# Performance work log

Hardware: AMD Instinct MI355X
Metric: run time of the kernel (lower is better)

The kernel has to match this reference:

```python
import jax, jax.numpy as jnp
import numpy as np

N = 1_000_000          # number of query points
POINT_DIMS = 2         # (x, y) coordinates
NUM_EMB = 6572         # number of video frames
EMB_DIM = 32
HIDDEN = 128


def setup_inputs() -> dict:
    key = jax.random.key(0)
    ks = jax.random.split(key, 10)
    x = jax.random.uniform(ks[0], (N, POINT_DIMS), dtype=jnp.float32)
    # fractional frame index in [0, NUM_EMB - 1)
    embeddings = jax.random.uniform(ks[1], (N,), dtype=jnp.float32) * (NUM_EMB - 1)
    em_table = jax.random.normal(ks[2], (NUM_EMB, EMB_DIM), dtype=jnp.float32) * 0.1
    in0 = POINT_DIMS + EMB_DIM
    W0 = jax.random.normal(ks[3], (in0, HIDDEN), dtype=jnp.float32) / np.sqrt(in0)
    b0 = jax.random.normal(ks[4], (HIDDEN,), dtype=jnp.float32) * 0.01
    W1 = jax.random.normal(ks[5], (HIDDEN, HIDDEN), dtype=jnp.float32) / np.sqrt(HIDDEN)
    b1 = jax.random.normal(ks[6], (HIDDEN,), dtype=jnp.float32) * 0.01
    W2 = jax.random.normal(ks[7], (HIDDEN, 1), dtype=jnp.float32) / np.sqrt(HIDDEN)
    b2 = jax.random.normal(ks[8], (1,), dtype=jnp.float32) * 0.01
    return {"x": x, "embeddings": embeddings, "em_table": em_table,
            "W0": W0, "b0": b0, "W1": W1, "b1": b1, "W2": W2, "b2": b2}


def reference(x, embeddings, em_table, W0, b0, W1, b1, W2, b2):
    num_emb = em_table.shape[0]
    em1 = embeddings.astype(jnp.int32)                       # floor (inputs >= 0)
    em2 = jnp.minimum(em1 + 1, num_emb - 1)                  # clamp(em1+1, max=E-1)
    res = (embeddings - em1.astype(jnp.float32))[:, None]    # [N, 1]
    e1 = em_table[em1]                                       # [N, 32] gather
    e2 = em_table[em2]                                       # [N, 32] gather
    em = e1 + (e2 - e1) * res                                # lerp
    h = jnp.concatenate((x, em), axis=1) @ W0 + b0           # [N, 128]
    h = jnp.clip(h, 0.0, 1.0)
    h = jnp.clip(h @ W1 + b1, 0.0, 1.0)
    out = jax.nn.sigmoid(h @ W2 + b2)                        # [N, 1]
    return out
```

## Files before the change

### kernel.cpp

```cpp
#include <hip/hip_runtime.h>
#include <hip/hip_bf16.h>


using bf16x8 = __attribute__((ext_vector_type(8))) short;
using f32x4  = __attribute__((ext_vector_type(4))) float;

#define NPTS    1000000
#define NUMEMB  6572
#define HID     128
#define M_IT    64
#define A0S     72
#define H0S     136
#define TILES   (NPTS / M_IT)
#define NBLOCKS 1024

__device__ __forceinline__ unsigned short bf16r(float f) {
    unsigned u;
    __builtin_memcpy(&u, &f, 4);
    u = (u + 0x7fffu + ((u >> 16) & 1u)) >> 16;
    return (unsigned short)u;
}
__device__ __forceinline__ unsigned pk2(float a, float b) {
    float2 f2; f2.x = a; f2.y = b;
    __hip_bfloat162 h = __float22bfloat162_rn(f2);
    unsigned u;
    __builtin_memcpy(&u, &h, 4);
    return u;
}
__device__ __forceinline__ float clamp01(float x) {
    return __builtin_amdgcn_fmed3f(x, 0.f, 1.f);
}

__global__ __launch_bounds__(256, 4)
void mlp_fused(const float* __restrict__ x,
               const float* __restrict__ emb,
               const float* __restrict__ em_table,
               const float* __restrict__ W0, const float* __restrict__ b0,
               const float* __restrict__ W1, const float* __restrict__ b1,
               const float* __restrict__ W2, const float* __restrict__ b2,
               float* __restrict__ out)
{
    __shared__ __align__(16) unsigned short A0[2 * M_IT * A0S];
    __shared__ __align__(16) unsigned short H0[M_IT * H0S];
    __shared__ __align__(16) float PART[16][65];

    const int tid  = threadIdx.x;
    const int lane = tid & 63;
    const int nq   = tid >> 6;
    const int q    = lane >> 4;
    const int cl   = lane & 15;
    const int p    = tid >> 2;
    const int s    = tid & 3;

    for (int i = tid; i < 2 * M_IT * A0S; i += 256) A0[i] = 0;

    const int hcol = nq * 32 + (cl >> 2) * 8 + (cl & 3);
    bf16x8 w0t[2][2];
    for (int hb = 0; hb < 2; ++hb)
        for (int kt = 0; kt < 2; ++kt) {
            const int col = hcol + hb * 4;
            bf16x8 v;
            #pragma unroll
            for (int e = 0; e < 8; ++e) {
                const int k = kt * 32 + q * 8 + e;
                float val = 0.f;
                if (k < 32)       val = W0[(2 + k) * HID + col];
                else if (k == 32) val = W0[0 * HID + col];
                else if (k == 33) val = W0[1 * HID + col];
                v[e] = (short)bf16r(val);
            }
            w0t[hb][kt] = v;
        }

    bf16x8 w1r[2][4];
    for (int hb = 0; hb < 2; ++hb)
        for (int kk = 0; kk < 4; ++kk) {
            const int kt  = (nq + kk) & 3;
            const int col = hcol + hb * 4;
            bf16x8 v;
            #pragma unroll
            for (int e = 0; e < 8; ++e) {
                const int k = kt * 32 + q * 8 + e;
                v[e] = (short)bf16r(W1[k * HID + col]);
            }
            w1r[hb][kk] = v;
        }

    f32x4 b0q[2], b1q[2], w2q[2];
    for (int hb = 0; hb < 2; ++hb)
        for (int r = 0; r < 4; ++r) {
            const int h = nq * 32 + q * 8 + hb * 4 + r;
            b0q[hb][r] = b0[h];
            b1q[hb][r] = b1[h];
            w2q[hb][r] = W2[h];
        }
    const float bias2 = b2[0];

    int t = blockIdx.x;
    int cur = 0;
    {
        const int gp = t * M_IT + p;
        const float fe = emb[gp];
        float2 xv = {0.f, 0.f};
        if (s == 0) xv = *(const float2*)(x + 2 * gp);
        const int e1 = (int)fe;
        const int e2 = (e1 + 1 < NUMEMB) ? e1 + 1 : NUMEMB - 1;
        const float r = fe - (float)e1;
        const float4* p1 = (const float4*)(em_table + e1 * 32 + s * 8);
        const float4* p2 = (const float4*)(em_table + e2 * 32 + s * 8);
        const float4 g0 = p1[0], g1 = p1[1], g2 = p2[0], g3 = p2[1];
        uint4 d;
        d.x = pk2(g0.x + (g2.x - g0.x) * r, g0.y + (g2.y - g0.y) * r);
        d.y = pk2(g0.z + (g2.z - g0.z) * r, g0.w + (g2.w - g0.w) * r);
        d.z = pk2(g1.x + (g3.x - g1.x) * r, g1.y + (g3.y - g1.y) * r);
        d.w = pk2(g1.z + (g3.z - g1.z) * r, g1.w + (g3.w - g1.w) * r);
        *(uint4*)&A0[p * A0S + s * 8] = d;
        if (s == 0) *(unsigned*)&A0[p * A0S + 32] = pk2(xv.x, xv.y);
    }
    float  feB;
    float2 xvB = {0.f, 0.f};
    {
        int t1 = t + gridDim.x; if (t1 >= TILES) t1 = t;
        const int gp = t1 * M_IT + p;
        feB = emb[gp];
        if (s == 0) xvB = *(const float2*)(x + 2 * gp);
    }

    __syncthreads();

    for (; t < TILES; t += gridDim.x, cur ^= 1) {
        const int base = t * M_IT;
        const unsigned short* A0c = A0 + cur * (M_IT * A0S);
        unsigned short*       A0n = A0 + (cur ^ 1) * (M_IT * A0S);

        f32x4 acc[4][2];
        #pragma unroll
        for (int pb = 0; pb < 4; ++pb) {
            #pragma unroll
            for (int kt = 0; kt < 2; ++kt) {
                bf16x8 bfrag = *(const bf16x8*)
                    &A0c[(pb * 16 + cl) * A0S + kt * 32 + q * 8];
                #pragma unroll
                for (int hb = 0; hb < 2; ++hb)
                    acc[pb][hb] = __builtin_amdgcn_mfma_f32_16x16x32_bf16(
                        w0t[hb][kt], bfrag,
                        (kt == 0) ? b0q[hb] : acc[pb][hb], 0, 0, 0);
            }
        }

        const int ge1 = (int)feB;
        const int ge2 = (ge1 + 1 < NUMEMB) ? ge1 + 1 : NUMEMB - 1;
        const float4* gp1 = (const float4*)(em_table + ge1 * 32 + s * 8);
        const float4* gp2 = (const float4*)(em_table + ge2 * 32 + s * 8);
        const float4 g0 = gp1[0], g1 = gp1[1], g2 = gp2[0], g3 = gp2[1];

        uint4 own[4];
        #pragma unroll
        for (int pb = 0; pb < 4; ++pb) {
            const f32x4 v0 = acc[pb][0], v1 = acc[pb][1];
            uint4 w;
            w.x = pk2(clamp01(v0[0]), clamp01(v0[1]));
            w.y = pk2(clamp01(v0[2]), clamp01(v0[3]));
            w.z = pk2(clamp01(v1[0]), clamp01(v1[1]));
            w.w = pk2(clamp01(v1[2]), clamp01(v1[3]));
            own[pb] = w;
            *(uint4*)&H0[(pb * 16 + cl) * H0S + nq * 32 + q * 8] = w;
        }

        {
            const float r = feB - (float)ge1;
            uint4 d;
            d.x = pk2(g0.x + (g2.x - g0.x) * r, g0.y + (g2.y - g0.y) * r);
            d.y = pk2(g0.z + (g2.z - g0.z) * r, g0.w + (g2.w - g0.w) * r);
            d.z = pk2(g1.x + (g3.x - g1.x) * r, g1.y + (g3.y - g1.y) * r);
            d.w = pk2(g1.z + (g3.z - g1.z) * r, g1.w + (g3.w - g1.w) * r);
            *(uint4*)&A0n[p * A0S + s * 8] = d;
            if (s == 0) *(unsigned*)&A0n[p * A0S + 32] = pk2(xvB.x, xvB.y);
        }
        {
            int t2 = t + 2 * (int)gridDim.x; if (t2 >= TILES) t2 = t;
            const int gp = t2 * M_IT + p;
            feB = emb[gp];
            if (s == 0) xvB = *(const float2*)(x + 2 * gp);
        }
        __syncthreads();

        #pragma unroll
        for (int pb = 0; pb < 4; ++pb) {
            bf16x8 bfrag;
            __builtin_memcpy(&bfrag, &own[pb], 16);
            #pragma unroll
            for (int hb = 0; hb < 2; ++hb)
                acc[pb][hb] = __builtin_amdgcn_mfma_f32_16x16x32_bf16(
                    w1r[hb][0], bfrag, b1q[hb], 0, 0, 0);
        }
        #pragma unroll
        for (int kk = 1; kk < 4; ++kk) {
            const int kcol = (((nq + kk) & 3) << 5) + q * 8;
            #pragma unroll
            for (int pb = 0; pb < 4; ++pb) {
                bf16x8 bfrag = *(const bf16x8*)
                    &H0[(pb * 16 + cl) * H0S + kcol];
                #pragma unroll
                for (int hb = 0; hb < 2; ++hb)
                    acc[pb][hb] = __builtin_amdgcn_mfma_f32_16x16x32_bf16(
                        w1r[hb][kk], bfrag, acc[pb][hb], 0, 0, 0);
            }
        }

        #pragma unroll
        for (int pb = 0; pb < 4; ++pb) {
            float sum = 0.f;
            #pragma unroll
            for (int hb = 0; hb < 2; ++hb) {
                const f32x4 v = acc[pb][hb];
                sum += clamp01(v[0]) * w2q[hb][0];
                sum += clamp01(v[1]) * w2q[hb][1];
                sum += clamp01(v[2]) * w2q[hb][2];
                sum += clamp01(v[3]) * w2q[hb][3];
            }
            PART[nq * 4 + q][pb * 16 + cl] = sum;
        }
        __syncthreads();

        if (tid < 64) {
            float z = bias2;
            #pragma unroll
            for (int i = 0; i < 16; ++i) z += PART[i][tid];
            out[base + tid] = 1.f / (1.f + __expf(-z));
        }
    }
}

extern "C" void kernel_launch(void* const* d_in, const int* in_sizes, int n_in,
                              void* d_out, int out_size, void* d_ws, size_t ws_size,
                              hipStream_t stream) {
    const float* x   = (const float*)d_in[0];
    const float* emb = (const float*)d_in[1];
    const float* emt = (const float*)d_in[2];
    const float* W0  = (const float*)d_in[3];
    const float* b0  = (const float*)d_in[4];
    const float* W1  = (const float*)d_in[5];
    const float* b1  = (const float*)d_in[6];
    const float* W2  = (const float*)d_in[7];
    const float* b2  = (const float*)d_in[8];
    mlp_fused<<<NBLOCKS, 256, 0, stream>>>(x, emb, emt, W0, b0, W1, b1, W2, b2,
                                           (float*)d_out);
}
```

Baseline: 133.5 us.

## Double per-block tile to 128 points and halve grid size

Grows each block's tile from 64 to 128 points. Every wave now runs 8 point-blocks per tile, which doubles the MFMA work done between barriers and amortises the per-tile sync and weight-register setup. The grid drops to 512 blocks and occupancy is lowered to 2 blocks per CU to fit the larger accumulators and LDS. Bounds clamping handles the partial last tile. The risk is higher register pressure and fewer resident waves to hide gather latency.

```diff
diff --git a/kernel.cpp b/kernel.cpp
--- a/kernel.cpp
+++ b/kernel.cpp
@@ -8,11 +8,11 @@
 #define NPTS    1000000
 #define NUMEMB  6572
 #define HID     128
-#define M_IT    64
+#define M_IT    128
 #define A0S     72
 #define H0S     136
-#define TILES   (NPTS / M_IT)
-#define NBLOCKS 1024
+#define TILES   ((NPTS + M_IT - 1) / M_IT)
+#define NBLOCKS 512
 
 __device__ __forceinline__ unsigned short bf16r(float f) {
     unsigned u;
@@ -31,7 +31,25 @@
     return __builtin_amdgcn_fmed3f(x, 0.f, 1.f);
 }
 
-__global__ __launch_bounds__(256, 4)
+__device__ __forceinline__ void stage_one(unsigned short* dst,
+                                          const float* __restrict__ em_table,
+                                          float fe, float2 xv, int s) {
+    const int e1 = (int)fe;
+    const int e2 = (e1 + 1 < NUMEMB) ? e1 + 1 : NUMEMB - 1;
+    const float r = fe - (float)e1;
+    const float4* p1 = (const float4*)(em_table + e1 * 32 + s * 8);
+    const float4* p2 = (const float4*)(em_table + e2 * 32 + s * 8);
+    const float4 g0 = p1[0], g1 = p1[1], g2 = p2[0], g3 = p2[1];
+    uint4 d;
+    d.x = pk2(g0.x + (g2.x - g0.x) * r, g0.y + (g2.y - g0.y) * r);
+    d.y = pk2(g0.z + (g2.z - g0.z) * r, g0.w + (g2.w - g0.w) * r);
+    d.z = pk2(g1.x + (g3.x - g1.x) * r, g1.y + (g3.y - g1.y) * r);
+    d.w = pk2(g1.z + (g3.z - g1.z) * r, g1.w + (g3.w - g1.w) * r);
+    *(uint4*)(dst + s * 8) = d;
+    if (s == 0) *(unsigned*)(dst + 32) = pk2(xv.x, xv.y);
+}
+
+__global__ __launch_bounds__(256, 2)
 void mlp_fused(const float* __restrict__ x,
                const float* __restrict__ emb,
                const float* __restrict__ em_table,
@@ -42,7 +60,7 @@
 {
     __shared__ __align__(16) unsigned short A0[2 * M_IT * A0S];
     __shared__ __align__(16) unsigned short H0[M_IT * H0S];
-    __shared__ __align__(16) float PART[16][65];
+    __shared__ __align__(16) float PART[16][M_IT + 1];
 
     const int tid  = threadIdx.x;
     const int lane = tid & 63;
@@ -99,31 +117,24 @@
     int t = blockIdx.x;
     int cur = 0;
     {
-        const int gp = t * M_IT + p;
-        const float fe = emb[gp];
-        float2 xv = {0.f, 0.f};
-        if (s == 0) xv = *(const float2*)(x + 2 * gp);
-        const int e1 = (int)fe;
-        const int e2 = (e1 + 1 < NUMEMB) ? e1 + 1 : NUMEMB - 1;
-        const float r = fe - (float)e1;
-        const float4* p1 = (const float4*)(em_table + e1 * 32 + s * 8);
-        const float4* p2 = (const float4*)(em_table + e2 * 32 + s * 8);
-        const float4 g0 = p1[0], g1 = p1[1], g2 = p2[0], g3 = p2[1];
-        uint4 d;
-        d.x = pk2(g0.x + (g2.x - g0.x) * r, g0.y + (g2.y - g0.y) * r);
-        d.y = pk2(g0.z + (g2.z - g0.z) * r, g0.w + (g2.w - g0.w) * r);
-        d.z = pk2(g1.x + (g3.x - g1.x) * r, g1.y + (g3.y - g1.y) * r);
-        d.w = pk2(g1.z + (g3.z - g1.z) * r, g1.w + (g3.w - g1.w) * r);
-        *(uint4*)&A0[p * A0S + s * 8] = d;
-        if (s == 0) *(unsigned*)&A0[p * A0S + 32] = pk2(xv.x, xv.y);
+        int gp0 = t * M_IT + p;        if (gp0 >= NPTS) gp0 = NPTS - 1;
+        int gp1 = t * M_IT + 64 + p;   if (gp1 >= NPTS) gp1 = NPTS - 1;
+        const float fe0 = emb[gp0], fe1 = emb[gp1];
+        float2 xv0 = {0.f, 0.f}, xv1 = {0.f, 0.f};
+        if (s == 0) { xv0 = *(const float2*)(x + 2 * gp0);
+                      xv1 = *(const float2*)(x + 2 * gp1); }
+        stage_one(&A0[p * A0S], em_table, fe0, xv0, s);
+        stage_one(&A0[(64 + p) * A0S], em_table, fe1, xv1, s);
     }
-    float  feB;
-    float2 xvB = {0.f, 0.f};
+    float  feB0, feB1;
+    float2 xvB0 = {0.f, 0.f}, xvB1 = {0.f, 0.f};
     {
         int t1 = t + gridDim.x; if (t1 >= TILES) t1 = t;
-        const int gp = t1 * M_IT + p;
-        feB = emb[gp];
-        if (s == 0) xvB = *(const float2*)(x + 2 * gp);
+        int gp0 = t1 * M_IT + p;      if (gp0 >= NPTS) gp0 = NPTS - 1;
+        int gp1 = t1 * M_IT + 64 + p; if (gp1 >= NPTS) gp1 = NPTS - 1;
+        feB0 = emb[gp0]; feB1 = emb[gp1];
+        if (s == 0) { xvB0 = *(const float2*)(x + 2 * gp0);
+                      xvB1 = *(const float2*)(x + 2 * gp1); }
     }
 
     __syncthreads();
@@ -133,9 +144,9 @@
         const unsigned short* A0c = A0 + cur * (M_IT * A0S);
         unsigned short*       A0n = A0 + (cur ^ 1) * (M_IT * A0S);
 
-        f32x4 acc[4][2];
-        #pragma unroll
-        for (int pb = 0; pb < 4; ++pb) {
+        f32x4 acc[8][2];
+        #pragma unroll
+        for (int pb = 0; pb < 8; ++pb) {
             #pragma unroll
             for (int kt = 0; kt < 2; ++kt) {
                 bf16x8 bfrag = *(const bf16x8*)
@@ -148,15 +159,15 @@
             }
         }
 
-        const int ge1 = (int)feB;
+        const int ge1 = (int)feB0;
         const int ge2 = (ge1 + 1 < NUMEMB) ? ge1 + 1 : NUMEMB - 1;
-        const float4* gp1 = (const float4*)(em_table + ge1 * 32 + s * 8);
-        const float4* gp2 = (const float4*)(em_table + ge2 * 32 + s * 8);
-        const float4 g0 = gp1[0], g1 = gp1[1], g2 = gp2[0], g3 = gp2[1];
-
-        uint4 own[4];
-        #pragma unroll
-        for (int pb = 0; pb < 4; ++pb) {
+        const float4* gp1p = (const float4*)(em_table + ge1 * 32 + s * 8);
+        const float4* gp2p = (const float4*)(em_table + ge2 * 32 + s * 8);
+        const float4 g0 = gp1p[0], g1 = gp1p[1], g2 = gp2p[0], g3 = gp2p[1];
+
+        uint4 own[8];
+        #pragma unroll
+        for (int pb = 0; pb < 8; ++pb) {
             const f32x4 v0 = acc[pb][0], v1 = acc[pb][1];
             uint4 w;
             w.x = pk2(clamp01(v0[0]), clamp01(v0[1]));
@@ -168,25 +179,29 @@
         }
 
         {
-            const float r = feB - (float)ge1;
+            const float r = feB0 - (float)ge1;
             uint4 d;
             d.x = pk2(g0.x + (g2.x - g0.x) * r, g0.y + (g2.y - g0.y) * r);
             d.y = pk2(g0.z + (g2.z - g0.z) * r, g0.w + (g2.w - g0.w) * r);
             d.z = pk2(g1.x + (g3.x - g1.x) * r, g1.y + (g3.y - g1.y) * r);
             d.w = pk2(g1.z + (g3.z - g1.z) * r, g1.w + (g3.w - g1.w) * r);
             *(uint4*)&A0n[p * A0S + s * 8] = d;
-            if (s == 0) *(unsigned*)&A0n[p * A0S + 32] = pk2(xvB.x, xvB.y);
-        }
+            if (s == 0) *(unsigned*)&A0n[p * A0S + 32] = pk2(xvB0.x, xvB0.y);
+        }
+        stage_one(&A0n[(64 + p) * A0S], em_table, feB1, xvB1, s);
+
         {
             int t2 = t + 2 * (int)gridDim.x; if (t2 >= TILES) t2 = t;
-            const int gp = t2 * M_IT + p;
-            feB = emb[gp];
-            if (s == 0) xvB = *(const float2*)(x + 2 * gp);
+            int gp0 = t2 * M_IT + p;      if (gp0 >= NPTS) gp0 = NPTS - 1;
+            int gpb = t2 * M_IT + 64 + p; if (gpb >= NPTS) gpb = NPTS - 1;
+            feB0 = emb[gp0]; feB1 = emb[gpb];
+            if (s == 0) { xvB0 = *(const float2*)(x + 2 * gp0);
+                          xvB1 = *(const float2*)(x + 2 * gpb); }
         }
         __syncthreads();
 
         #pragma unroll
-        for (int pb = 0; pb < 4; ++pb) {
+        for (int pb = 0; pb < 8; ++pb) {
             bf16x8 bfrag;
             __builtin_memcpy(&bfrag, &own[pb], 16);
             #pragma unroll
@@ -198,7 +213,7 @@
         for (int kk = 1; kk < 4; ++kk) {
             const int kcol = (((nq + kk) & 3) << 5) + q * 8;
             #pragma unroll
-            for (int pb = 0; pb < 4; ++pb) {
+            for (int pb = 0; pb < 8; ++pb) {
                 bf16x8 bfrag = *(const bf16x8*)
                     &H0[(pb * 16 + cl) * H0S + kcol];
                 #pragma unroll
@@ -209,7 +224,7 @@
         }
 
         #pragma unroll
-        for (int pb = 0; pb < 4; ++pb) {
+        for (int pb = 0; pb < 8; ++pb) {
             float sum = 0.f;
             #pragma unroll
             for (int hb = 0; hb < 2; ++hb) {
@@ -223,11 +238,14 @@
         }
         __syncthreads();
 
-        if (tid < 64) {
-            float z = bias2;
-            #pragma unroll
-            for (int i = 0; i < 16; ++i) z += PART[i][tid];
-            out[base + tid] = 1.f / (1.f + __expf(-z));
+        if (tid < 128) {
+            const int gp = base + tid;
+            if (gp < NPTS) {
+                float z = bias2;
+                #pragma unroll
+                for (int i = 0; i < 16; ++i) z += PART[i][tid];
+                out[gp] = 1.f / (1.f + __expf(-z));
+            }
         }
     }
 }
```

After: 134.1 us. About the same (+0.4%).
